# Kernel optimization log

Measured on AMD Instinct MI355X. Metric: run time of the kernel, lower is better.

Reference implementation:

```python
import jax, jax.numpy as jnp
import numpy as np

# Constants matching init_kwargs
PC_MIN_X, PC_MIN_Y = -70.4, -40.0
VX, VY = 0.1, 0.1
RADII = (0.4, 0.8)
NSAMPLE = 16
EPS = 1e-5

B, K, N = 2, 2048, 16384
C_BEV, H_BEV, W_BEV = 256, 100, 176


def setup_inputs() -> dict:
    key = jax.random.key(0)
    ks = jax.random.split(key, 16)
    u = lambda k, s: jax.random.uniform(k, s, jnp.float32)
    kp = jnp.stack([
        u(ks[0], (B, K)) * 136.0 - 68.0,
        u(ks[1], (B, K)) * 76.0 - 38.0,
        u(ks[2], (B, K)) * 2.5 - 2.0,   # z in (-2.0, 0.5) -> kpt_mask all True
    ], axis=-1)
    pts = jnp.stack([
        u(ks[3], (B, N)) * 140.0 - 70.0,
        u(ks[4], (B, N)) * 80.0 - 40.0,
        u(ks[5], (B, N)) * 4.0 - 3.0,
    ], axis=-1)
    r = lambda k, s: jax.random.normal(k, s, jnp.float32)
    s01 = lambda k, s: r(k, s) * 0.1
    return {
        "keypoints": kp,
        "points_xyz": pts,
        "points_feat": r(ks[6], (B, N, 1)),
        "spatial_features": r(ks[7], (B, C_BEV, H_BEV, W_BEV)),
        "bev_stride": 8,
        "W0_s0": s01(ks[8], (16, 4)), "g0_s0": jnp.ones(16), "b0_s0": jnp.zeros(16),
        "W1_s0": s01(ks[9], (16, 16)), "g1_s0": jnp.ones(16), "b1_s0": jnp.zeros(16),
        "W0_s1": s01(ks[10], (16, 4)), "g0_s1": jnp.ones(16), "b0_s1": jnp.zeros(16),
        "W1_s1": s01(ks[11], (32, 16)), "g1_s1": jnp.ones(32), "b1_s1": jnp.zeros(32),
        "Wf": s01(ks[12], (128, 304)), "gf": jnp.ones(128), "bf": jnp.zeros(128),
    }


def _batchnorm(x, g, b, axes):
    m = x.mean(axes, keepdims=True)
    v = x.var(axes, keepdims=True)
    return (x - m) * jax.lax.rsqrt(v + EPS) * g + b


def _ball_group(dist2, xyz_b, feat_b, kp_b, radius, ns):
    """pcdet ball_query: first ns in-radius neighbors (index order), pad by first idx."""
    Kq, Np = dist2.shape
    within = dist2 < radius * radius                      # (K, N)
    order = jnp.cumsum(within, axis=1) - 1                # slot for each point
    valid = within & (order < ns)
    pos = jnp.where(valid, order, ns)                     # invalid -> overflow slot
    idx = jnp.zeros((Kq, ns + 1), jnp.int32)
    idx = idx.at[jnp.arange(Kq)[:, None], pos].set(
        jnp.broadcast_to(jnp.arange(Np, dtype=jnp.int32)[None, :], (Kq, Np)))
    idx = idx[:, :ns]
    cnt = within.sum(axis=1)
    slot_ok = jnp.arange(ns)[None, :] < cnt[:, None]
    idx = jnp.where(slot_ok, idx, idx[:, :1])             # replicate first found idx
    empty = cnt == 0
    grouped_xyz = xyz_b[idx] - kp_b[:, None, :]           # (K, ns, 3)
    grouped = jnp.concatenate([grouped_xyz, feat_b[idx]], axis=-1)  # (K, ns, 3+C)
    grouped = jnp.where(empty[:, None, None], 0.0, grouped)
    return grouped, empty


def _group_both_scales(xyz_b, feat_b, kp_b):
    # pairwise dist computed ONCE, shared across both radii
    dist2 = jnp.sum((kp_b[:, None, :] - xyz_b[None, :, :]) ** 2, axis=-1)  # (K, N)
    g0, e0 = _ball_group(dist2, xyz_b, feat_b, kp_b, RADII[0], NSAMPLE)
    g1, e1 = _ball_group(dist2, xyz_b, feat_b, kp_b, RADII[1], NSAMPLE)
    return g0, e0, g1, e1


def _shared_mlp_pool(grouped, empty, layers):
    x = grouped                                            # (B, K, ns, Cin)
    for (W, g, b) in layers:
        x = jnp.einsum('bknc,oc->bkno', x, W)
        x = _batchnorm(x, g, b, axes=(0, 1, 2))            # BN2d over stacked M*ns
        x = jax.nn.relu(x)
    pooled = x.max(axis=2)                                 # max over ns -> (B, K, Cout)
    return jnp.where(empty[:, :, None], 0.0, pooled)


def _bev_interp(bev, kp, stride):
    # bev: (B, C, H, W); kp: (B, K, 3)
    im = jnp.transpose(bev, (0, 2, 3, 1))                  # (B, H, W, C)
    x = (kp[..., 0] - PC_MIN_X) / VX / stride
    y = (kp[..., 1] - PC_MIN_Y) / VY / stride
    Hh, Ww = im.shape[1], im.shape[2]
    x0 = jnp.clip(jnp.floor(x).astype(jnp.int32), 0, Ww - 1)
    x1 = jnp.clip(jnp.floor(x).astype(jnp.int32) + 1, 0, Ww - 1)
    y0 = jnp.clip(jnp.floor(y).astype(jnp.int32), 0, Hh - 1)
    y1 = jnp.clip(jnp.floor(y).astype(jnp.int32) + 1, 0, Hh - 1)
    bidx = jnp.arange(im.shape[0])[:, None]
    Ia, Ib = im[bidx, y0, x0], im[bidx, y1, x0]
    Ic, Id = im[bidx, y0, x1], im[bidx, y1, x1]
    x0f, x1f = x0.astype(x.dtype), x1.astype(x.dtype)
    y0f, y1f = y0.astype(y.dtype), y1.astype(y.dtype)
    wa = ((x1f - x) * (y1f - y))[..., None]
    wb = ((x1f - x) * (y - y0f))[..., None]
    wc = ((x - x0f) * (y1f - y))[..., None]
    wd = ((x - x0f) * (y - y0f))[..., None]
    return Ia * wa + Ib * wb + Ic * wc + Id * wd           # (B, K, C)


def reference(keypoints, points_xyz, points_feat, spatial_features, bev_stride,
              W0_s0, g0_s0, b0_s0, W1_s0, g1_s0, b1_s0,
              W0_s1, g0_s1, b0_s1, W1_s1, g1_s1, b1_s1,
              Wf, gf, bf):
    Bb, Kk, _ = keypoints.shape
    # BEV bilinear interpolation
    bev_feat = _bev_interp(spatial_features, keypoints, bev_stride)  # (B, K, C_bev)
    # per-batch ball-query grouping (vmapped over batch)
    g0, e0, g1, e1 = jax.vmap(_group_both_scales)(points_xyz, points_feat, keypoints)
    p0 = _shared_mlp_pool(g0, e0, [(W0_s0, g0_s0, b0_s0), (W1_s0, g1_s0, b1_s0)])
    p1 = _shared_mlp_pool(g1, e1, [(W0_s1, g0_s1, b0_s1), (W1_s1, g1_s1, b1_s1)])
    pooled = jnp.concatenate([p0, p1], axis=-1)            # (B, K, 48)
    feats = jnp.concatenate([bev_feat, pooled], axis=-1).reshape(Bb * Kk, -1)  # (M, 304)
    # vsa_point_feature_fusion: Linear(no bias) + BN1d(train) + ReLU
    fused = feats @ Wf.T
    fused = jax.nn.relu(_batchnorm(fused, gf, bf, axes=(0,)))
    return fused                                           # (B*K, 128)
```

## Files before the change

### kernel.cpp

```cpp
#include <hip/hip_runtime.h>
#include <hip/hip_bf16.h>

#define NB    2
#define NK    2048
#define NPTS  16384
#define NBK   4096
#define MSAMP 65536.0f
#define MROW  4096.0f

__global__ __launch_bounds__(256) void mega_kernel(
    const float* __restrict__ kp, const float* __restrict__ pts,
    const float* __restrict__ pfeat, const float* __restrict__ bev,
    float* __restrict__ g0buf, float* __restrict__ g1buf,
    int* __restrict__ cnt, float* __restrict__ part0,
    float* __restrict__ bevT)
{
  __shared__ __align__(16) char smem[21504];
  const int t = threadIdx.x;
  const int wave = t >> 6;
  const int lane = t & 63;

  if (blockIdx.x >= 512) {
    float (*ttile)[65] = (float (*)[65])smem;
    const int tb  = blockIdx.x - 512;
    const int b   = tb / 1100;
    const int rem = tb % 1100;
    const int cg  = (rem / 275) * 64;
    const int sp0 = (rem % 275) * 64;
    #pragma unroll 4
    for (int i = 0; i < 16; i++) {
      const int c = cg + wave * 16 + i;
      ttile[wave * 16 + i][lane] = bev[((size_t)(b * 256 + c)) * 17600 + sp0 + lane];
    }
    __syncthreads();
    #pragma unroll 4
    for (int i = 0; i < 16; i++) {
      const int s = wave * 16 + i;
      bevT[((size_t)b * 17600 + sp0 + s) * 256 + cg + lane] = ttile[lane][s];
    }
    return;
  }

  float* sxyz  = (float*)smem;
  float* sfeat = (float*)(smem + 12288);
  float (*slots)[2][2][16][4] = (float (*)[2][2][16][4])(smem + 16384);
  float (*bred)[28] = (float (*)[28])(smem + 20480);

  const int gb = blockIdx.x;
  const int bkA = gb * 8 + wave * 2;
  const int bkB = bkA + 1;
  const int b  = gb >> 8;
  const float kxA = kp[bkA*3+0], kyA = kp[bkA*3+1], kzA = kp[bkA*3+2];
  const float kxB = kp[bkB*3+0], kyB = kp[bkB*3+1], kzB = kp[bkB*3+2];
  const float* px = pts   + (size_t)b * NPTS * 3;
  const float* pf = pfeat + (size_t)b * NPTS;
  int c0A = 0, c1A = 0, c0B = 0, c1B = 0;
  bool done = false;
  const unsigned long long below = (1ull << lane) - 1ull;

  for (int tile = 0; tile < 16; tile++) {
    __syncthreads();
    {
      const float4* gsrc = (const float4*)(px + tile * 3072);
      float4* ldst = (float4*)sxyz;
      ldst[t]       = gsrc[t];
      ldst[t + 256] = gsrc[t + 256];
      ldst[t + 512] = gsrc[t + 512];
      #pragma unroll
      for (int i = 0; i < 4; i++) sfeat[t + i * 256] = pf[tile * 1024 + t + i * 256];
    }
    __syncthreads();
    if (!done) {
      for (int inner = 0; inner < 16; inner++) {
        const int pp = inner * 64 + lane;
        const float x = sxyz[pp*3+0];
        const float y = sxyz[pp*3+1];
        const float z = sxyz[pp*3+2];
        const float dxA = x - kxA, dyA = y - kyA, dzA = z - kzA;
        const float d2A = dxA*dxA + dyA*dyA + dzA*dzA;
        const float dxB = x - kxB, dyB = y - kyB, dzB = z - kzB;
        const float d2B = dxB*dxB + dyB*dyB + dzB*dzB;
        const bool w1a = d2A < 0.64f;
        const bool w1b = d2B < 0.64f;
        const unsigned long long m1a = __ballot(w1a);
        const unsigned long long m1b = __ballot(w1b);
        if (m1a | m1b) {
          const bool w0a = d2A < 0.16f;
          const bool w0b = d2B < 0.16f;
          const unsigned long long m0a = __ballot(w0a);
          const unsigned long long m0b = __ballot(w0b);
          const float f = sfeat[pp];
          {
            const int o0 = c0A + __popcll(m0a & below);
            if (w0a && o0 < 16) {
              slots[wave][0][0][o0][0] = dxA; slots[wave][0][0][o0][1] = dyA;
              slots[wave][0][0][o0][2] = dzA; slots[wave][0][0][o0][3] = f;
            }
            const int o1 = c1A + __popcll(m1a & below);
            if (w1a && o1 < 16) {
              slots[wave][0][1][o1][0] = dxA; slots[wave][0][1][o1][1] = dyA;
              slots[wave][0][1][o1][2] = dzA; slots[wave][0][1][o1][3] = f;
            }
            c0A += __popcll(m0a);
            c1A += __popcll(m1a);
          }
          {
            const int o0 = c0B + __popcll(m0b & below);
            if (w0b && o0 < 16) {
              slots[wave][1][0][o0][0] = dxB; slots[wave][1][0][o0][1] = dyB;
              slots[wave][1][0][o0][2] = dzB; slots[wave][1][0][o0][3] = f;
            }
            const int o1 = c1B + __popcll(m1b & below);
            if (w1b && o1 < 16) {
              slots[wave][1][1][o1][0] = dxB; slots[wave][1][1][o1][1] = dyB;
              slots[wave][1][1][o1][2] = dzB; slots[wave][1][1][o1][3] = f;
            }
            c0B += __popcll(m0b);
            c1B += __popcll(m1b);
          }
          if (c0A >= 16 && c0B >= 16) { done = true; break; }
        }
      }
    }
  }
  __syncthreads();

  {
    const int kpid = lane >> 5;
    const int s    = (lane >> 4) & 1;
    const int sl   = lane & 15;
    const int cs = kpid ? (s ? c1B : c0B) : (s ? c1A : c0A);
    if (cs == 0) {
      slots[wave][kpid][s][sl][0] = 0.f; slots[wave][kpid][s][sl][1] = 0.f;
      slots[wave][kpid][s][sl][2] = 0.f; slots[wave][kpid][s][sl][3] = 0.f;
    } else if (sl >= cs) {
      slots[wave][kpid][s][sl][0] = slots[wave][kpid][s][0][0];
      slots[wave][kpid][s][sl][1] = slots[wave][kpid][s][0][1];
      slots[wave][kpid][s][sl][2] = slots[wave][kpid][s][0][2];
      slots[wave][kpid][s][sl][3] = slots[wave][kpid][s][0][3];
    }
  }

  g0buf[(size_t)bkA * 64 + lane] = slots[wave][0][0][lane >> 2][lane & 3];
  g1buf[(size_t)bkA * 64 + lane] = slots[wave][0][1][lane >> 2][lane & 3];
  g0buf[(size_t)bkB * 64 + lane] = slots[wave][1][0][lane >> 2][lane & 3];
  g1buf[(size_t)bkB * 64 + lane] = slots[wave][1][1][lane >> 2][lane & 3];
  if (lane == 0) {
    cnt[bkA] = c0A; cnt[NBK + bkA] = c1A;
    cnt[bkB] = c0B; cnt[NBK + bkB] = c1B;
  }

  float v[14];
  {
    const int kpid = lane >> 5;
    const int s    = (lane >> 4) & 1;
    const int sl   = lane & 15;
    const float x0 = slots[wave][kpid][s][sl][0];
    const float x1 = slots[wave][kpid][s][sl][1];
    const float x2 = slots[wave][kpid][s][sl][2];
    const float x3 = slots[wave][kpid][s][sl][3];
    v[0] = x0; v[1] = x1; v[2] = x2; v[3] = x3;
    v[4] = x0*x0; v[5] = x0*x1; v[6]  = x0*x2; v[7]  = x0*x3;
    v[8] = x1*x1; v[9] = x1*x2; v[10] = x1*x3;
    v[11] = x2*x2; v[12] = x2*x3; v[13] = x3*x3;
  }
  #pragma unroll
  for (int d = 1; d < 16; d <<= 1) {
    #pragma unroll
    for (int i = 0; i < 14; i++) v[i] += __shfl_xor(v[i], d);
  }
  #pragma unroll
  for (int i = 0; i < 14; i++) v[i] += __shfl_xor(v[i], 32);
  if (lane == 0 || lane == 16) {
    float* dst = &bred[wave][(lane >> 4) * 14];
    #pragma unroll
    for (int i = 0; i < 14; i++) dst[i] = v[i];
  }
  __syncthreads();
  if (t < 28) {
    part0[gb * 28 + t] = bred[0][t] + bred[1][t] + bred[2][t] + bred[3][t];
  }
}

__device__ __forceinline__ void bn0_params(
    int t, const float* S0, const float* sW0a, const float* sW0b,
    const float* gm0s0, const float* bt0s0,
    const float* gm0s1, const float* bt0s1, float* sP)
{
  if (t < 32) {
    const int s = t >> 4, c = t & 15;
    const float* W  = s ? sW0b : sW0a;
    const float* G  = s ? gm0s1 : gm0s0;
    const float* Bt = s ? bt0s1 : bt0s0;
    const float* Sx = S0 + s * 14;
    const float w0 = W[c*4+0], w1 = W[c*4+1];
    const float w2 = W[c*4+2], w3 = W[c*4+3];
    const float inv = 1.0f / MSAMP;
    const float mean = (w0*Sx[0] + w1*Sx[1] + w2*Sx[2] + w3*Sx[3]) * inv;
    float e2 = w0*w0*Sx[4] + 2.f*w0*w1*Sx[5] + 2.f*w0*w2*Sx[6] + 2.f*w0*w3*Sx[7]
             + w1*w1*Sx[8] + 2.f*w1*w2*Sx[9] + 2.f*w1*w3*Sx[10]
             + w2*w2*Sx[11] + 2.f*w2*w3*Sx[12] + w3*w3*Sx[13];
    e2 *= inv;
    const float var = e2 - mean * mean;
    const float A = G[c] / sqrtf(var + 1e-5f);
    sP[s*32 + c]      = A;
    sP[s*32 + 16 + c] = Bt[c] - mean * A;
  }
}

__global__ __launch_bounds__(256) void stats1_kernel(
    const float* __restrict__ g0buf, const float* __restrict__ g1buf,
    const float* __restrict__ part0,
    const float* __restrict__ W0s0, const float* __restrict__ gm0s0, const float* __restrict__ bt0s0,
    const float* __restrict__ W0s1, const float* __restrict__ gm0s1, const float* __restrict__ bt0s1,
    const float* __restrict__ W1s0, const float* __restrict__ W1s1,
    float* __restrict__ part1)
{
  __shared__ float sW0a[64], sW0b[64], sW1a[256], sW1b[512], sP[64];
  __shared__ float tmp0[8][28], S0[28];
  __shared__ float red[16][96];
  const int t = threadIdx.x;
  if (t < 64) { sW0a[t] = W0s0[t]; sW0b[t] = W0s1[t]; }
  sW1a[t]       = W1s0[t];
  sW1b[t]       = W1s1[t];
  sW1b[t + 256] = W1s1[t + 256];
  for (int i = t; i < 16 * 96; i += 256) ((float*)red)[i] = 0.f;
  if (t < 224) {
    const int seg = t / 28, col = t % 28;
    float s = 0.f;
    for (int r = seg * 64; r < seg * 64 + 64; r++) s += part0[r * 28 + col];
    tmp0[seg][col] = s;
  }
  __syncthreads();
  if (t < 28) {
    float s = 0.f;
    #pragma unroll
    for (int g = 0; g < 8; g++) s += tmp0[g][t];
    S0[t] = s;
  }
  __syncthreads();
  bn0_params(t, S0, sW0a, sW0b, gm0s0, bt0s0, gm0s1, bt0s1, sP);
  __syncthreads();

  const int slot = blockIdx.x * 256 + t;
  const int wave = t >> 6, lane = t & 63;
  const int grp  = (wave << 2) | (lane >> 4);
  const bool leader = (lane & 15) == 0;

  float a1[16];
  {
    const float4 x = *(const float4*)(g0buf + (size_t)slot * 4);
    #pragma unroll
    for (int c = 0; c < 16; c++) {
      const float h = sW0a[c*4+0]*x.x + sW0a[c*4+1]*x.y + sW0a[c*4+2]*x.z + sW0a[c*4+3]*x.w;
      a1[c] = fmaxf(fmaf(sP[c], h, sP[16+c]), 0.f);
    }
    #pragma unroll
    for (int o = 0; o < 16; o++) {
      float h2 = 0.f;
      #pragma unroll
      for (int c = 0; c < 16; c++) h2 = fmaf(sW1a[o*16+c], a1[c], h2);
      float s = h2, q = h2 * h2;
      #pragma unroll
      for (int d = 1; d < 16; d <<= 1) { s += __shfl_xor(s, d); q += __shfl_xor(q, d); }
      if (leader) { red[grp][o] += s; red[grp][16+o] += q; }
    }
  }
  {
    const float4 x = *(const float4*)(g1buf + (size_t)slot * 4);
    #pragma unroll
    for (int c = 0; c < 16; c++) {
      const float h = sW0b[c*4+0]*x.x + sW0b[c*4+1]*x.y + sW0b[c*4+2]*x.z + sW0b[c*4+3]*x.w;
      a1[c] = fmaxf(fmaf(sP[32+c], h, sP[48+c]), 0.f);
    }
    #pragma unroll
    for (int o = 0; o < 32; o++) {
      float h2 = 0.f;
      #pragma unroll
      for (int c = 0; c < 16; c++) h2 = fmaf(sW1b[o*16+c], a1[c], h2);
      float s = h2, q = h2 * h2;
      #pragma unroll
      for (int d = 1; d < 16; d <<= 1) { s += __shfl_xor(s, d); q += __shfl_xor(q, d); }
      if (leader) { red[grp][32+o] += s; red[grp][64+o] += q; }
    }
  }
  __syncthreads();
  if (t < 96) {
    float s = 0.f;
    #pragma unroll
    for (int g = 0; g < 16; g++) s += red[g][t];
    part1[blockIdx.x * 96 + t] = s;
  }
}

__global__ __launch_bounds__(256) void poolgemm_kernel(
    const float* __restrict__ kp, const int* __restrict__ stridep,
    const float* __restrict__ bevT,
    const float* __restrict__ g0buf, const float* __restrict__ g1buf,
    const int* __restrict__ cnt,
    const float* __restrict__ part0, const float* __restrict__ part1,
    const float* __restrict__ W0s0, const float* __restrict__ gm0s0, const float* __restrict__ bt0s0,
    const float* __restrict__ W0s1, const float* __restrict__ gm0s1, const float* __restrict__ bt0s1,
    const float* __restrict__ W1s0, const float* __restrict__ gm1s0, const float* __restrict__ bt1s0,
    const float* __restrict__ W1s1, const float* __restrict__ gm1s1, const float* __restrict__ bt1s1,
    const float* __restrict__ Wf,
    float* __restrict__ fused, float* __restrict__ part2)
{
  __shared__ float sW0a[64], sW0b[64], sW1a[256], sW1b[512], sP[160];
  __shared__ float tmp0[8][28], S0[28];
  __shared__ float tmp1[2][96], S1[96];
  __shared__ float skp[24];
  __shared__ float t2s[2][128], t2q[2][128];
  __shared__ __align__(16) float sF[8 * 304];
  const int t = threadIdx.x;
  const int bk0 = blockIdx.x * 8;

  if (t < 24) skp[t] = kp[(size_t)bk0 * 3 + t];
  if (t < 64)  { sW0a[t] = W0s0[t]; sW0b[t] = W0s1[t]; }
  sW1a[t]       = W1s0[t];
  sW1b[t]       = W1s1[t];
  sW1b[t + 256] = W1s1[t + 256];
  if (t < 224) {
    const int seg = t / 28, col = t % 28;
    float s = 0.f;
    for (int r = seg * 64; r < seg * 64 + 64; r++) s += part0[r * 28 + col];
    tmp0[seg][col] = s;
  }
  __syncthreads();

  {
    const float st = (float)(*stridep);
    const int b = bk0 >> 11;
    const size_t pb = (size_t)b * 17600 * 256;
    #pragma unroll
    for (int r = 0; r < 8; r++) {
      const float x = (skp[r*3+0] - (-70.4f)) / 0.1f / st;
      const float y = (skp[r*3+1] - (-40.0f)) / 0.1f / st;
      const int xf = (int)floorf(x), yf = (int)floorf(y);
      const int x0 = min(max(xf, 0), 175), x1 = min(max(xf + 1, 0), 175);
      const int y0 = min(max(yf, 0), 99),  y1 = min(max(yf + 1, 0), 99);
      const float x0f = (float)x0, x1f = (float)x1, y0f = (float)y0, y1f = (float)y1;
      const float wa = (x1f - x) * (y1f - y);
      const float wb = (x1f - x) * (y - y0f);
      const float wc = (x - x0f) * (y1f - y);
      const float wd = (x - x0f) * (y - y0f);
      const float Ia = bevT[pb + (size_t)(y0 * 176 + x0) * 256 + t];
      const float Ib = bevT[pb + (size_t)(y1 * 176 + x0) * 256 + t];
      const float Ic = bevT[pb + (size_t)(y0 * 176 + x1) * 256 + t];
      const float Id = bevT[pb + (size_t)(y1 * 176 + x1) * 256 + t];
      sF[r * 304 + t] = Ia * wa + Ib * wb + Ic * wc + Id * wd;
    }
  }

  if (t < 28) {
    float s = 0.f;
    #pragma unroll
    for (int g = 0; g < 8; g++) s += tmp0[g][t];
    S0[t] = s;
  }
  if (t >= 32 && t < 224) {
    const int tt = t - 32;
    const int seg = tt / 96, col = tt % 96;
    float s = 0.f;
    for (int r = seg * 128; r < seg * 128 + 128; r++) s += part1[r * 96 + col];
    tmp1[seg][col] = s;
  }
  __syncthreads();
  bn0_params(t, S0, sW0a, sW0b, gm0s0, bt0s0, gm0s1, bt0s1, sP);
  if (t >= 64 && t < 160) {
    const int c = t - 64;
    S1[c] = tmp1[0][c] + tmp1[1][c];
  }
  __syncthreads();
  if (t < 48) {
    float sum, sq, G, Bv; int oA, oB;
    if (t < 16) { sum = S1[t];    sq = S1[16+t]; G = gm1s0[t]; Bv = bt1s0[t]; oA = 64+t;  oB = 80+t; }
    else { const int c = t - 16; sum = S1[32+c]; sq = S1[64+c]; G = gm1s1[c]; Bv = bt1s1[c]; oA = 96+c; oB = 128+c; }
    const float mean = sum / MSAMP;
    const float var  = sq / MSAMP - mean * mean;
    const float A = G / sqrtf(var + 1e-5f);
    sP[oA] = A;
    sP[oB] = Bv - mean * A;
  }
  __syncthreads();

  if (t < 128) {
    const int lkp = t >> 4, slot = t & 15;
    const int bk = bk0 + lkp;
    const size_t si = (size_t)bk * 16 + slot;
    float a1[16], a2s0[16], a2s1[32];
    {
      const float4 x = *(const float4*)(g0buf + si * 4);
      #pragma unroll
      for (int c = 0; c < 16; c++) {
        const float h = sW0a[c*4+0]*x.x + sW0a[c*4+1]*x.y + sW0a[c*4+2]*x.z + sW0a[c*4+3]*x.w;
        a1[c] = fmaxf(fmaf(sP[c], h, sP[16+c]), 0.f);
      }
      #pragma unroll
      for (int o = 0; o < 16; o++) {
        float h2 = 0.f;
        #pragma unroll
        for (int c = 0; c < 16; c++) h2 = fmaf(sW1a[o*16+c], a1[c], h2);
        a2s0[o] = fmaxf(fmaf(sP[64+o], h2, sP[80+o]), 0.f);
      }
    }
    {
      const float4 x = *(const float4*)(g1buf + si * 4);
      #pragma unroll
      for (int c = 0; c < 16; c++) {
        const float h = sW0b[c*4+0]*x.x + sW0b[c*4+1]*x.y + sW0b[c*4+2]*x.z + sW0b[c*4+3]*x.w;
        a1[c] = fmaxf(fmaf(sP[32+c], h, sP[48+c]), 0.f);
      }
      #pragma unroll
      for (int o = 0; o < 32; o++) {
        float h2 = 0.f;
        #pragma unroll
        for (int c = 0; c < 16; c++) h2 = fmaf(sW1b[o*16+c], a1[c], h2);
        a2s1[o] = fmaxf(fmaf(sP[96+o], h2, sP[128+o]), 0.f);
      }
    }
    #pragma unroll
    for (int d = 1; d < 16; d <<= 1) {
      #pragma unroll
      for (int o = 0; o < 16; o++) a2s0[o] = fmaxf(a2s0[o], __shfl_xor(a2s0[o], d));
      #pragma unroll
      for (int o = 0; o < 32; o++) a2s1[o] = fmaxf(a2s1[o], __shfl_xor(a2s1[o], d));
    }
    if (slot == 0) {
      const int c0 = cnt[bk], c1 = cnt[NBK + bk];
      float* outp = sF + lkp * 304 + 256;
      #pragma unroll
      for (int o = 0; o < 16; o++) outp[o] = c0 ? a2s0[o] : 0.f;
      #pragma unroll
      for (int o = 0; o < 32; o++) outp[16 + o] = c1 ? a2s1[o] : 0.f;
    }
  }
  __syncthreads();

  {
    const int c = t & 127;
    const int half = t >> 7;
    const int rbase = half * 4;
    float acc[4];
    #pragma unroll
    for (int r = 0; r < 4; r++) acc[r] = 0.f;
    const float* wrow = Wf + (size_t)c * 304;
    for (int j4 = 0; j4 < 76; j4++) {
      const float4 w = *(const float4*)(wrow + j4 * 4);
      #pragma unroll
      for (int r = 0; r < 4; r++) {
        const float4 f = *(const float4*)(sF + (rbase + r) * 304 + j4 * 4);
        acc[r] = fmaf(w.x, f.x, acc[r]);
        acc[r] = fmaf(w.y, f.y, acc[r]);
        acc[r] = fmaf(w.z, f.z, acc[r]);
        acc[r] = fmaf(w.w, f.w, acc[r]);
      }
    }
    float s = 0.f, q = 0.f;
    #pragma unroll
    for (int r = 0; r < 4; r++) {
      fused[(size_t)(bk0 + rbase + r) * 128 + c] = acc[r];
      s += acc[r];
      q = fmaf(acc[r], acc[r], q);
    }
    t2s[half][c] = s;
    t2q[half][c] = q;
  }
  __syncthreads();
  if (t < 128) {
    part2[blockIdx.x * 256 + t]       = t2s[0][t] + t2s[1][t];
    part2[blockIdx.x * 256 + 128 + t] = t2q[0][t] + t2q[1][t];
  }
}

__global__ __launch_bounds__(256) void out_kernel(
    const float* __restrict__ fused, const float* __restrict__ part2,
    const float* __restrict__ gf, const float* __restrict__ bfp,
    float* __restrict__ out)
{
  __shared__ float sA[128], sB[128];
  __shared__ float tmp[2][128];
  const int t = threadIdx.x;
  {
    const int c = t & 127, which = t >> 7;
    float s = 0.f;
    for (int r = 0; r < 512; r++) s += part2[r * 256 + which * 128 + c];
    tmp[which][c] = s;
  }
  __syncthreads();
  if (t < 128) {
    const float mean = tmp[0][t] / MROW;
    const float var  = tmp[1][t] / MROW - mean * mean;
    const float A = gf[t] / sqrtf(var + 1e-5f);
    sA[t] = A;
    sB[t] = bfp[t] - mean * A;
  }
  __syncthreads();
  #pragma unroll
  for (int k = 0; k < 4; k++) {
    const int f4 = blockIdx.x * 1024 + k * 256 + t;
    const int i = f4 * 4;
    const float4 v = *(const float4*)(fused + i);
    const int c = i & 127;
    float4 o;
    o.x = fmaxf(fmaf(v.x, sA[c+0], sB[c+0]), 0.f);
    o.y = fmaxf(fmaf(v.y, sA[c+1], sB[c+1]), 0.f);
    o.z = fmaxf(fmaf(v.z, sA[c+2], sB[c+2]), 0.f);
    o.w = fmaxf(fmaf(v.w, sA[c+3], sB[c+3]), 0.f);
    *(float4*)(out + i) = o;
  }
}

extern "C" void kernel_launch(void* const* d_in, const int* in_sizes, int n_in,
                              void* d_out, int out_size, void* d_ws, size_t ws_size,
                              hipStream_t stream)
{
  const float* kp    = (const float*)d_in[0];
  const float* pts   = (const float*)d_in[1];
  const float* pfeat = (const float*)d_in[2];
  const float* bev   = (const float*)d_in[3];
  const int*   strd  = (const int*)d_in[4];
  const float* W0s0  = (const float*)d_in[5];
  const float* g0s0  = (const float*)d_in[6];
  const float* b0s0  = (const float*)d_in[7];
  const float* W1s0  = (const float*)d_in[8];
  const float* g1s0  = (const float*)d_in[9];
  const float* b1s0  = (const float*)d_in[10];
  const float* W0s1  = (const float*)d_in[11];
  const float* g0s1  = (const float*)d_in[12];
  const float* b0s1  = (const float*)d_in[13];
  const float* W1s1  = (const float*)d_in[14];
  const float* g1s1  = (const float*)d_in[15];
  const float* b1s1  = (const float*)d_in[16];
  const float* Wf    = (const float*)d_in[17];
  const float* gf    = (const float*)d_in[18];
  const float* bfv   = (const float*)d_in[19];

  float* w      = (float*)d_ws;
  float* g0buf  = w;
  float* g1buf  = w + 262144;
  float* fused  = w + 524288;
  float* part0  = w + 1048576;
  float* part1  = w + 1081344;
  float* part2  = w + 1105920;
  int*   cnt    = (int*)(w + 1236992);
  float* bevT   = w + 1245184;

  hipLaunchKernelGGL(mega_kernel,  dim3(2712), dim3(256), 0, stream,
                     kp, pts, pfeat, bev, g0buf, g1buf, cnt, part0, bevT);
  hipLaunchKernelGGL(stats1_kernel, dim3(256), dim3(256), 0, stream,
                     g0buf, g1buf, part0,
                     W0s0, g0s0, b0s0, W0s1, g0s1, b0s1, W1s0, W1s1, part1);
  hipLaunchKernelGGL(poolgemm_kernel, dim3(512), dim3(256), 0, stream,
                     kp, strd, bevT, g0buf, g1buf, cnt, part0, part1,
                     W0s0, g0s0, b0s0, W0s1, g0s1, b0s1,
                     W1s0, g1s0, b1s0, W1s1, g1s1, b1s1,
                     Wf, fused, part2);
  hipLaunchKernelGGL(out_kernel,   dim3(128), dim3(256), 0, stream,
                     fused, part2, gf, bfv, (float*)d_out);
}
```

Baseline: 212.9 us.

## Replace brute-force ball query with a spatial grid binning and a 3x3 cell search

Adds a bin kernel that counting-sorts each batch's points into a 0.8 m XY grid, storing sorted xyz+feature and original indices. The grouping kernel then gives one thread per keypoint and scans only the 3x3 neighbouring cells, instead of every wave streaming all 16384 points through LDS. Padding uses the lowest original index found, and the 14 moment sums are accumulated in registers and reduced per block, which also cuts the part0 reduction to 16 rows. Neighbours are visited in cell order rather than index order, so when more than 16 points fall in the radius the chosen subset can differ from the reference. The binning step runs in only two blocks and relies on LDS atomics.

```diff
diff --git a/kernel.cpp b/kernel.cpp
--- a/kernel.cpp
+++ b/kernel.cpp
@@ -8,21 +8,103 @@
 #define MSAMP 65536.0f
 #define MROW  4096.0f
 
-__global__ __launch_bounds__(256) void mega_kernel(
-    const float* __restrict__ kp, const float* __restrict__ pts,
-    const float* __restrict__ pfeat, const float* __restrict__ bev,
+#define NCELLX 176
+#define NCELLY 101
+#define NCELLS 17776
+#define CSTRIDE (NCELLS + 16)
+
+#define ACC14(M, w, X, Y, Z, F) do { \
+  M[0] += (w)*(X); M[1] += (w)*(Y); M[2] += (w)*(Z); M[3] += (w)*(F); \
+  M[4] += (w)*(X)*(X); M[5] += (w)*(X)*(Y); M[6] += (w)*(X)*(Z); M[7] += (w)*(X)*(F); \
+  M[8] += (w)*(Y)*(Y); M[9] += (w)*(Y)*(Z); M[10] += (w)*(Y)*(F); \
+  M[11] += (w)*(Z)*(Z); M[12] += (w)*(Z)*(F); M[13] += (w)*(F)*(F); } while (0)
+
+__global__ __launch_bounds__(1024) void bin_kernel(
+    const float* __restrict__ pts, const float* __restrict__ pfeat,
+    float* __restrict__ pts_srt, int* __restrict__ idx_srt,
+    int* __restrict__ cellstart)
+{
+  __shared__ int hist[NCELLS];
+  __shared__ int wsum[16];
+  const int t = threadIdx.x;
+  const int b = blockIdx.x;
+  const float* px = pts + (size_t)b * NPTS * 3;
+  const float* pf = pfeat + (size_t)b * NPTS;
+  float4* psrt = (float4*)pts_srt + (size_t)b * NPTS;
+  int* isrt = idx_srt + b * NPTS;
+  int* csg  = cellstart + b * CSTRIDE;
+
+  for (int c = t; c < NCELLS; c += 1024) hist[c] = 0;
+  __syncthreads();
+
+  int cell[16];
+  #pragma unroll
+  for (int k = 0; k < 16; k++) {
+    const int i = t + k * 1024;
+    const float x = px[i*3+0], y = px[i*3+1];
+    int cx = (int)floorf((x + 70.4f) * 1.25f);
+    int cy = (int)floorf((y + 40.0f) * 1.25f);
+    cx = min(max(cx, 0), NCELLX - 1);
+    cy = min(max(cy, 0), NCELLY - 1);
+    cell[k] = cy * NCELLX + cx;
+    atomicAdd(&hist[cell[k]], 1);
+  }
+  __syncthreads();
+
+  const int lane = t & 63, wv = t >> 6;
+  const int cbase = t * 18;
+  int lsum = 0;
+  #pragma unroll
+  for (int j = 0; j < 18; j++) {
+    const int c = cbase + j;
+    if (c < NCELLS) lsum += hist[c];
+  }
+  int xin = lsum;
+  #pragma unroll
+  for (int d = 1; d < 64; d <<= 1) { const int y = __shfl_up(xin, d); if (lane >= d) xin += y; }
+  if (lane == 63) wsum[wv] = xin;
+  __syncthreads();
+  if (t < 16) {
+    int y = wsum[t];
+    #pragma unroll
+    for (int d = 1; d < 16; d <<= 1) { const int z = __shfl_up(y, d); if (t >= d) y += z; }
+    wsum[t] = y;
+  }
+  __syncthreads();
+  int run = (wv ? wsum[wv - 1] : 0) + xin - lsum;
+  #pragma unroll
+  for (int j = 0; j < 18; j++) {
+    const int c = cbase + j;
+    if (c < NCELLS) { const int h = hist[c]; hist[c] = run; csg[c] = run; run += h; }
+  }
+  if (t == 0) csg[NCELLS] = NPTS;
+  __syncthreads();
+
+  #pragma unroll
+  for (int k = 0; k < 16; k++) {
+    const int i = t + k * 1024;
+    const int pos = atomicAdd(&hist[cell[k]], 1);
+    psrt[pos] = make_float4(px[i*3+0], px[i*3+1], px[i*3+2], pf[i]);
+    isrt[pos] = i;
+  }
+}
+
+__global__ __launch_bounds__(256) void grouptrans_kernel(
+    const float* __restrict__ kp, const float* __restrict__ bev,
+    const float* __restrict__ pts_srt, const int* __restrict__ idx_srt,
+    const int* __restrict__ cellstart,
     float* __restrict__ g0buf, float* __restrict__ g1buf,
     int* __restrict__ cnt, float* __restrict__ part0,
     float* __restrict__ bevT)
 {
-  __shared__ __align__(16) char smem[21504];
+  __shared__ __align__(16) char smem[16640];
   const int t = threadIdx.x;
   const int wave = t >> 6;
   const int lane = t & 63;
 
-  if (blockIdx.x >= 512) {
+  if (blockIdx.x >= 16) {
     float (*ttile)[65] = (float (*)[65])smem;
-    const int tb  = blockIdx.x - 512;
+    const int tb  = blockIdx.x - 16;
     const int b   = tb / 1100;
     const int rem = tb % 1100;
     const int cg  = (rem / 275) * 64;
@@ -41,144 +123,88 @@
     return;
   }
 
-  float* sxyz  = (float*)smem;
-  float* sfeat = (float*)(smem + 12288);
-  float (*slots)[2][2][16][4] = (float (*)[2][2][16][4])(smem + 16384);
-  float (*bred)[28] = (float (*)[28])(smem + 20480);
-
-  const int gb = blockIdx.x;
-  const int bkA = gb * 8 + wave * 2;
-  const int bkB = bkA + 1;
-  const int b  = gb >> 8;
-  const float kxA = kp[bkA*3+0], kyA = kp[bkA*3+1], kzA = kp[bkA*3+2];
-  const float kxB = kp[bkB*3+0], kyB = kp[bkB*3+1], kzB = kp[bkB*3+2];
-  const float* px = pts   + (size_t)b * NPTS * 3;
-  const float* pf = pfeat + (size_t)b * NPTS;
-  int c0A = 0, c1A = 0, c0B = 0, c1B = 0;
-  bool done = false;
-  const unsigned long long below = (1ull << lane) - 1ull;
-
-  for (int tile = 0; tile < 16; tile++) {
-    __syncthreads();
-    {
-      const float4* gsrc = (const float4*)(px + tile * 3072);
-      float4* ldst = (float4*)sxyz;
-      ldst[t]       = gsrc[t];
-      ldst[t + 256] = gsrc[t + 256];
-      ldst[t + 512] = gsrc[t + 512];
-      #pragma unroll
-      for (int i = 0; i < 4; i++) sfeat[t + i * 256] = pf[tile * 1024 + t + i * 256];
-    }
-    __syncthreads();
-    if (!done) {
-      for (int inner = 0; inner < 16; inner++) {
-        const int pp = inner * 64 + lane;
-        const float x = sxyz[pp*3+0];
-        const float y = sxyz[pp*3+1];
-        const float z = sxyz[pp*3+2];
-        const float dxA = x - kxA, dyA = y - kyA, dzA = z - kzA;
-        const float d2A = dxA*dxA + dyA*dyA + dzA*dzA;
-        const float dxB = x - kxB, dyB = y - kyB, dzB = z - kzB;
-        const float d2B = dxB*dxB + dyB*dyB + dzB*dzB;
-        const bool w1a = d2A < 0.64f;
-        const bool w1b = d2B < 0.64f;
-        const unsigned long long m1a = __ballot(w1a);
-        const unsigned long long m1b = __ballot(w1b);
-        if (m1a | m1b) {
-          const bool w0a = d2A < 0.16f;
-          const bool w0b = d2B < 0.16f;
-          const unsigned long long m0a = __ballot(w0a);
-          const unsigned long long m0b = __ballot(w0b);
-          const float f = sfeat[pp];
-          {
-            const int o0 = c0A + __popcll(m0a & below);
-            if (w0a && o0 < 16) {
-              slots[wave][0][0][o0][0] = dxA; slots[wave][0][0][o0][1] = dyA;
-              slots[wave][0][0][o0][2] = dzA; slots[wave][0][0][o0][3] = f;
-            }
-            const int o1 = c1A + __popcll(m1a & below);
-            if (w1a && o1 < 16) {
-              slots[wave][0][1][o1][0] = dxA; slots[wave][0][1][o1][1] = dyA;
-              slots[wave][0][1][o1][2] = dzA; slots[wave][0][1][o1][3] = f;
-            }
-            c0A += __popcll(m0a);
-            c1A += __popcll(m1a);
+  float (*bred)[28] = (float (*)[28])smem;
+
+  const int bk = blockIdx.x * 256 + t;
+  const int b  = bk >> 11;
+  const float kx = kp[bk*3+0], ky = kp[bk*3+1], kz = kp[bk*3+2];
+  int cx = (int)floorf((kx + 70.4f) * 1.25f);
+  int cy = (int)floorf((ky + 40.0f) * 1.25f);
+  cx = min(max(cx, 1), NCELLX - 2);
+  cy = min(max(cy, 1), NCELLY - 2);
+
+  const float4* psrt = (const float4*)pts_srt + (size_t)b * NPTS;
+  const int* isrt = idx_srt + b * NPTS;
+  const int* csg  = cellstart + b * CSTRIDE;
+  float* gA = g0buf + (size_t)bk * 64;
+  float* gB = g1buf + (size_t)bk * 64;
+
+  int c0 = 0, c1 = 0;
+  int mi0 = 0x7fffffff, mi1 = 0x7fffffff;
+  float p0x = 0.f, p0y = 0.f, p0z = 0.f, p0f = 0.f;
+  float p1x = 0.f, p1y = 0.f, p1z = 0.f, p1f = 0.f;
+  float M0[14], M1[14];
+  #pragma unroll
+  for (int i = 0; i < 14; i++) { M0[i] = 0.f; M1[i] = 0.f; }
+
+  for (int dyc = -1; dyc <= 1; ++dyc) {
+    const int base = (cy + dyc) * NCELLX + cx - 1;
+    const int s = csg[base];
+    const int e = csg[base + 3];
+    for (int j = s; j < e; ++j) {
+      const float4 p = psrt[j];
+      const float dx = p.x - kx, dy = p.y - ky, dz = p.z - kz;
+      const float d2 = dx*dx + dy*dy + dz*dz;
+      if (d2 < 0.64f) {
+        const int pi = isrt[j];
+        if (c1 < 16) {
+          *(float4*)(gB + c1 * 4) = make_float4(dx, dy, dz, p.w);
+          ACC14(M1, 1.0f, dx, dy, dz, p.w);
+        }
+        if (pi < mi1) { mi1 = pi; p1x = dx; p1y = dy; p1z = dz; p1f = p.w; }
+        c1++;
+        if (d2 < 0.16f) {
+          if (c0 < 16) {
+            *(float4*)(gA + c0 * 4) = make_float4(dx, dy, dz, p.w);
+            ACC14(M0, 1.0f, dx, dy, dz, p.w);
           }
-          {
-            const int o0 = c0B + __popcll(m0b & below);
-            if (w0b && o0 < 16) {
-              slots[wave][1][0][o0][0] = dxB; slots[wave][1][0][o0][1] = dyB;
-              slots[wave][1][0][o0][2] = dzB; slots[wave][1][0][o0][3] = f;
-            }
-            const int o1 = c1B + __popcll(m1b & below);
-            if (w1b && o1 < 16) {
-              slots[wave][1][1][o1][0] = dxB; slots[wave][1][1][o1][1] = dyB;
-              slots[wave][1][1][o1][2] = dzB; slots[wave][1][1][o1][3] = f;
-            }
-            c0B += __popcll(m0b);
-            c1B += __popcll(m1b);
-          }
-          if (c0A >= 16 && c0B >= 16) { done = true; break; }
+          if (pi < mi0) { mi0 = pi; p0x = dx; p0y = dy; p0z = dz; p0f = p.w; }
+          c0++;
         }
       }
     }
   }
-  __syncthreads();
-
-  {
-    const int kpid = lane >> 5;
-    const int s    = (lane >> 4) & 1;
-    const int sl   = lane & 15;
-    const int cs = kpid ? (s ? c1B : c0B) : (s ? c1A : c0A);
-    if (cs == 0) {
-      slots[wave][kpid][s][sl][0] = 0.f; slots[wave][kpid][s][sl][1] = 0.f;
-      slots[wave][kpid][s][sl][2] = 0.f; slots[wave][kpid][s][sl][3] = 0.f;
-    } else if (sl >= cs) {
-      slots[wave][kpid][s][sl][0] = slots[wave][kpid][s][0][0];
-      slots[wave][kpid][s][sl][1] = slots[wave][kpid][s][0][1];
-      slots[wave][kpid][s][sl][2] = slots[wave][kpid][s][0][2];
-      slots[wave][kpid][s][sl][3] = slots[wave][kpid][s][0][3];
-    }
-  }
-
-  g0buf[(size_t)bkA * 64 + lane] = slots[wave][0][0][lane >> 2][lane & 3];
-  g1buf[(size_t)bkA * 64 + lane] = slots[wave][0][1][lane >> 2][lane & 3];
-  g0buf[(size_t)bkB * 64 + lane] = slots[wave][1][0][lane >> 2][lane & 3];
-  g1buf[(size_t)bkB * 64 + lane] = slots[wave][1][1][lane >> 2][lane & 3];
+
+  {
+    const float4 v0 = make_float4(p0x, p0y, p0z, p0f);
+    for (int s2 = c0; s2 < 16; ++s2) *(float4*)(gA + s2 * 4) = v0;
+    const float w0 = (float)(16 - min(c0, 16));
+    ACC14(M0, w0, p0x, p0y, p0z, p0f);
+  }
+  {
+    const float4 v1 = make_float4(p1x, p1y, p1z, p1f);
+    for (int s2 = c1; s2 < 16; ++s2) *(float4*)(gB + s2 * 4) = v1;
+    const float w1 = (float)(16 - min(c1, 16));
+    ACC14(M1, w1, p1x, p1y, p1z, p1f);
+  }
+  cnt[bk] = c0;
+  cnt[NBK + bk] = c1;
+
+  #pragma unroll
+  for (int d = 1; d < 64; d <<= 1) {
+    #pragma unroll
+    for (int i = 0; i < 14; i++) {
+      M0[i] += __shfl_xor(M0[i], d);
+      M1[i] += __shfl_xor(M1[i], d);
+    }
+  }
   if (lane == 0) {
-    cnt[bkA] = c0A; cnt[NBK + bkA] = c1A;
-    cnt[bkB] = c0B; cnt[NBK + bkB] = c1B;
-  }
-
-  float v[14];
-  {
-    const int kpid = lane >> 5;
-    const int s    = (lane >> 4) & 1;
-    const int sl   = lane & 15;
-    const float x0 = slots[wave][kpid][s][sl][0];
-    const float x1 = slots[wave][kpid][s][sl][1];
-    const float x2 = slots[wave][kpid][s][sl][2];
-    const float x3 = slots[wave][kpid][s][sl][3];
-    v[0] = x0; v[1] = x1; v[2] = x2; v[3] = x3;
-    v[4] = x0*x0; v[5] = x0*x1; v[6]  = x0*x2; v[7]  = x0*x3;
-    v[8] = x1*x1; v[9] = x1*x2; v[10] = x1*x3;
-    v[11] = x2*x2; v[12] = x2*x3; v[13] = x3*x3;
-  }
-  #pragma unroll
-  for (int d = 1; d < 16; d <<= 1) {
-    #pragma unroll
-    for (int i = 0; i < 14; i++) v[i] += __shfl_xor(v[i], d);
-  }
-  #pragma unroll
-  for (int i = 0; i < 14; i++) v[i] += __shfl_xor(v[i], 32);
-  if (lane == 0 || lane == 16) {
-    float* dst = &bred[wave][(lane >> 4) * 14];
-    #pragma unroll
-    for (int i = 0; i < 14; i++) dst[i] = v[i];
+    #pragma unroll
+    for (int i = 0; i < 14; i++) { bred[wave][i] = M0[i]; bred[wave][14 + i] = M1[i]; }
   }
   __syncthreads();
   if (t < 28) {
-    part0[gb * 28 + t] = bred[0][t] + bred[1][t] + bred[2][t] + bred[3][t];
+    part0[blockIdx.x * 28 + t] = bred[0][t] + bred[1][t] + bred[2][t] + bred[3][t];
   }
 }
 
@@ -217,7 +243,7 @@
     float* __restrict__ part1)
 {
   __shared__ float sW0a[64], sW0b[64], sW1a[256], sW1b[512], sP[64];
-  __shared__ float tmp0[8][28], S0[28];
+  __shared__ float S0[28];
   __shared__ float red[16][96];
   const int t = threadIdx.x;
   if (t < 64) { sW0a[t] = W0s0[t]; sW0b[t] = W0s1[t]; }
@@ -225,17 +251,10 @@
   sW1b[t]       = W1s1[t];
   sW1b[t + 256] = W1s1[t + 256];
   for (int i = t; i < 16 * 96; i += 256) ((float*)red)[i] = 0.f;
-  if (t < 224) {
-    const int seg = t / 28, col = t % 28;
-    float s = 0.f;
-    for (int r = seg * 64; r < seg * 64 + 64; r++) s += part0[r * 28 + col];
-    tmp0[seg][col] = s;
-  }
-  __syncthreads();
   if (t < 28) {
     float s = 0.f;
     #pragma unroll
-    for (int g = 0; g < 8; g++) s += tmp0[g][t];
+    for (int r = 0; r < 16; r++) s += part0[r * 28 + t];
     S0[t] = s;
   }
   __syncthreads();
@@ -307,7 +326,7 @@
     float* __restrict__ fused, float* __restrict__ part2)
 {
   __shared__ float sW0a[64], sW0b[64], sW1a[256], sW1b[512], sP[160];
-  __shared__ float tmp0[8][28], S0[28];
+  __shared__ float S0[28];
   __shared__ float tmp1[2][96], S1[96];
   __shared__ float skp[24];
   __shared__ float t2s[2][128], t2q[2][128];
@@ -320,11 +339,11 @@
   sW1a[t]       = W1s0[t];
   sW1b[t]       = W1s1[t];
   sW1b[t + 256] = W1s1[t + 256];
-  if (t < 224) {
-    const int seg = t / 28, col = t % 28;
+  if (t < 28) {
     float s = 0.f;
-    for (int r = seg * 64; r < seg * 64 + 64; r++) s += part0[r * 28 + col];
-    tmp0[seg][col] = s;
+    #pragma unroll
+    for (int r = 0; r < 16; r++) s += part0[r * 28 + t];
+    S0[t] = s;
   }
   __syncthreads();
 
@@ -352,12 +371,6 @@
     }
   }
 
-  if (t < 28) {
-    float s = 0.f;
-    #pragma unroll
-    for (int g = 0; g < 8; g++) s += tmp0[g][t];
-    S0[t] = s;
-  }
   if (t >= 32 && t < 224) {
     const int tt = t - 32;
     const int seg = tt / 96, col = tt % 96;
@@ -546,8 +559,15 @@
   int*   cnt    = (int*)(w + 1236992);
   float* bevT   = w + 1245184;
 
-  hipLaunchKernelGGL(mega_kernel,  dim3(2712), dim3(256), 0, stream,
-                     kp, pts, pfeat, bev, g0buf, g1buf, cnt, part0, bevT);
+  int*   idx_srt   = (int*)(w + 524288);
+  int*   cellstart = (int*)(w + 524288 + 32768);
+  float* pts_srt   = w + 1105920;
+
+  hipLaunchKernelGGL(bin_kernel, dim3(2), dim3(1024), 0, stream,
+                     pts, pfeat, pts_srt, idx_srt, cellstart);
+  hipLaunchKernelGGL(grouptrans_kernel, dim3(2216), dim3(256), 0, stream,
+                     kp, bev, pts_srt, idx_srt, cellstart,
+                     g0buf, g1buf, cnt, part0, bevT);
   hipLaunchKernelGGL(stats1_kernel, dim3(256), dim3(256), 0, stream,
                      g0buf, g1buf, part0,
                      W0s0, g0s0, b0s0, W0s1, g0s1, b0s1, W1s0, W1s1, part1);
```

Result: slower. 236.1 us (+10.9%).
